# Performance work log

Measured on AMD Instinct MI355X. Metric: run time of the kernel, lower is better.

## Reference

```python
import jax, jax.numpy as jnp
import numpy as np

N = 50000
E = 800000
D = 128          # in_dim = hidden_dim = out_dim
H = 4            # heads
C = D // H       # per-head channels = 32
L = 3            # num_layers
SLOPE = 0.2
BN_EPS = 1e-5


def setup_inputs() -> dict:
    key = jax.random.key(0)
    ks = jax.random.split(key, 12)
    x = jax.random.normal(ks[0], (N, D), dtype=jnp.float32)
    ei = jax.random.randint(ks[1], (2, E), 0, N, dtype=jnp.int64)
    # remove accidental self loops (PyG removes then re-adds them)
    src, dst = ei[0], ei[1]
    src = jnp.where(src == dst, (src + 1) % N, src)
    edge_index = jnp.stack([src, dst])
    s = 1.0 / np.sqrt(D)
    Wl = jax.random.normal(ks[2], (L, D, D), dtype=jnp.float32) * s
    Wr = jax.random.normal(ks[3], (L, D, D), dtype=jnp.float32) * s
    att = jax.random.normal(ks[4], (L, H, C), dtype=jnp.float32) * (1.0 / np.sqrt(C))
    bias = jnp.zeros((L, D), dtype=jnp.float32)
    Wres = jax.random.normal(ks[5], (L, D, D), dtype=jnp.float32) * s
    gamma = jnp.ones((L, D), dtype=jnp.float32)
    beta = jnp.zeros((L, D), dtype=jnp.float32)
    W_out = jax.random.normal(ks[6], (D, D), dtype=jnp.float32) * s
    b_out = jnp.zeros((D,), dtype=jnp.float32)
    return {"x": x, "edge_index": edge_index, "Wl": Wl, "Wr": Wr, "att": att,
            "bias": bias, "Wres": Wres, "gamma": gamma, "beta": beta,
            "W_out": W_out, "b_out": b_out}


def _segment_softmax(scores, seg, num_segments):
    # scores: [E, H], seg: [E] dst ids
    m = jax.ops.segment_max(scores, seg, num_segments=num_segments)  # [N, H]
    ex = jnp.exp(scores - m[seg])
    denom = jax.ops.segment_sum(ex, seg, num_segments=num_segments)  # [N, H]
    return ex / denom[seg]


def _gatv2_layer(x, src, dst, Wl_, Wr_, att_, b_, Wres_):
    xl = (x @ Wl_).reshape(N, H, C)   # source-side transform
    xr = (x @ Wr_).reshape(N, H, C)   # target-side transform
    msg = xl[src]                      # [E, H, C]
    pre = jax.nn.leaky_relu(msg + xr[dst], SLOPE)
    e = jnp.einsum('ehc,hc->eh', pre, att_)          # [E, H]
    alpha = _segment_softmax(e, dst, N)              # [E, H]
    agg = jax.ops.segment_sum(alpha[..., None] * msg, dst, num_segments=N)
    return agg.reshape(N, D) + b_ + x @ Wres_


def _batch_norm(x, g, b):
    mu = jnp.mean(x, axis=0)
    var = jnp.mean(jnp.square(x - mu), axis=0)  # biased, as in torch BN
    return (x - mu) * jax.lax.rsqrt(var + BN_EPS) * g + b


def reference(x, edge_index, Wl, Wr, att, bias, Wres, gamma, beta, W_out, b_out):
    # add self loops once (same augmentation every layer)
    loops = jnp.arange(N, dtype=edge_index.dtype)
    src = jnp.concatenate([edge_index[0], loops])
    dst = jnp.concatenate([edge_index[1], loops])
    for i in range(L):
        x = _gatv2_layer(x, src, dst, Wl[i], Wr[i], att[i], bias[i], Wres[i])
        x = _batch_norm(x, gamma[i], beta[i])
        x = jax.nn.leaky_relu(x, SLOPE)
        # dropout = identity in eval
    return x @ W_out + b_out
```

## Files before the change

### kernel.cpp

```cpp
#include <hip/hip_runtime.h>
#include <hip/hip_bf16.h>

constexpr int N = 50000;
constexpr int E = 800000;
constexpr int D = 128;
constexpr int H = 4;
constexpr int C = 32;
constexpr int L = 3;
constexpr int E2 = E + N;
constexpr float SLOPE = 0.2f;
constexpr float BN_EPS = 1e-5f;
constexpr float LOG2E = 1.4426950408889634f;
constexpr int TILES = (N + 63) / 64;
constexpr int NPART = 32;

typedef __attribute__((ext_vector_type(8))) short bf16x8_t;
typedef __attribute__((ext_vector_type(4))) float f32x4_t;
typedef __attribute__((ext_vector_type(2))) float v2f;

using hbf = __hip_bfloat16;

__device__ __forceinline__ float fast_exp2(float x) { return __builtin_amdgcn_exp2f(x); }

__device__ __forceinline__ short f2bf(float v) {
    hbf h = __float2bfloat16(v);
    return *reinterpret_cast<short*>(&h);
}
__device__ __forceinline__ v2f bfpair_to_v2(unsigned int u) {
    v2f r;
    r.x = __uint_as_float(u << 16);
    r.y = __uint_as_float(u & 0xffff0000u);
    return r;
}

__global__ void count_kernel(const int* __restrict__ ei, int* __restrict__ counts,
                             int* __restrict__ rank) {
    int i = blockIdx.x * blockDim.x + threadIdx.x;
    if (i >= E2) return;
    int dst = (i < E) ? ei[E + i] : (i - E);
    rank[i] = atomicAdd(&counts[dst], 1);
}

__global__ __launch_bounds__(512) void scan_block_kernel(const int* __restrict__ counts,
                                                         int* __restrict__ row_ptr,
                                                         int* __restrict__ blk_sums) {
    __shared__ int s[512];
    int t = threadIdx.x;
    int i = blockIdx.x * 512 + t;
    int v = (i < N) ? counts[i] : 0;
    s[t] = v;
    __syncthreads();
    for (int off = 1; off < 512; off <<= 1) {
        int add = (t >= off) ? s[t - off] : 0;
        __syncthreads();
        s[t] += add;
        __syncthreads();
    }
    if (i < N) row_ptr[i] = s[t] - v;
    if (t == 511) blk_sums[blockIdx.x] = s[511];
}

__global__ __launch_bounds__(128) void scan_sums_kernel(int* __restrict__ blk, int nb) {
    __shared__ int s[128];
    int t = threadIdx.x;
    int v = (t < nb) ? blk[t] : 0;
    s[t] = v;
    __syncthreads();
    for (int off = 1; off < 128; off <<= 1) {
        int add = (t >= off) ? s[t - off] : 0;
        __syncthreads();
        s[t] += add;
        __syncthreads();
    }
    if (t < nb) blk[t] = s[t] - v;
}

__global__ void scan_add_kernel(int* __restrict__ row_ptr, const int* __restrict__ blk) {
    int i = blockIdx.x * blockDim.x + threadIdx.x;
    if (i < N) row_ptr[i] += blk[i >> 9];
    if (i == 0) row_ptr[N] = E2;
}

__global__ void scatter_kernel(const int* __restrict__ ei, const int* __restrict__ row_ptr,
                               const int* __restrict__ rank, int* __restrict__ col_idx) {
    int i = blockIdx.x * blockDim.x + threadIdx.x;
    if (i >= E2) return;
    int src, dst;
    if (i < E) { src = ei[i]; dst = ei[E + i]; }
    else       { src = i - E; dst = i - E; }
    col_idx[row_ptr[dst] + rank[i]] = src;
}

__global__ __launch_bounds__(256) void pack_w_kernel(
        const float* __restrict__ Wl, const float* __restrict__ Wr,
        const float* __restrict__ Wres, const float* __restrict__ Wout,
        hbf* __restrict__ Wph) {
    int gid = blockIdx.x * 256 + threadIdx.x;
    int mat = gid >> 14;
    int d = gid & 16383;
    const float* W;
    if (mat < 3)      W = Wl + (size_t)mat * 16384;
    else if (mat < 6) W = Wr + (size_t)(mat - 3) * 16384;
    else if (mat < 9) W = Wres + (size_t)(mat - 6) * 16384;
    else              W = Wout;
    int j = d & 7, lane = (d >> 3) & 63, nb = (d >> 9) & 7, ks = d >> 12;
    int k = ks * 32 + ((lane >> 4) * 8) + j;
    int n = nb * 16 + (lane & 15);
    Wph[gid] = __float2bfloat16(W[k * D + n]);
}

__global__ __launch_bounds__(256) void gemm3_mfma_kernel(
        const float* x, const float* __restrict__ sums,
        const float* __restrict__ gamma, const float* __restrict__ beta,
        const hbf* __restrict__ Wph,
        int mL, int mR, int mS, const float* __restrict__ bias,
        hbf* __restrict__ xl, hbf* __restrict__ xr, float* y) {
    __shared__ hbf xsh[64][136];
    __shared__ hbf xsl[64][136];
    __shared__ float ssl[2][128];
    int t = threadIdx.x;
    int wave = t >> 6;
    int lane = t & 63;
    int nb0 = wave * 2;
    int row0 = blockIdx.x * 64;

    if (sums && t < 128) {
        float sm = 0.f, s2 = 0.f;
#pragma unroll 8
        for (int p = 0; p < NPART; ++p) {
            sm += sums[p * 256 + t];
            s2 += sums[p * 256 + 128 + t];
        }
        float mean = sm * (1.0f / N);
        float var = fmaxf(s2 * (1.0f / N) - mean * mean, 0.f);
        float sc = gamma[t] * rsqrtf(var + BN_EPS);
        ssl[0][t] = sc;
        ssl[1][t] = beta[t] - mean * sc;
    }

    const bf16x8_t* B = (const bf16x8_t*)Wph;
    bf16x8_t bL[4][2], bR[4][2], bS[4][2];
#pragma unroll
    for (int ks = 0; ks < 4; ++ks)
#pragma unroll
        for (int j = 0; j < 2; ++j) {
            int bo = (ks * 8 + nb0 + j) * 64 + lane;
            bL[ks][j] = B[mL * 2048 + bo];
            bR[ks][j] = B[mR * 2048 + bo];
            bS[ks][j] = B[mS * 2048 + bo];
        }
    __syncthreads();

    int cg = (t & 31) * 4;
    {
        float sc_[4] = {1.f, 1.f, 1.f, 1.f}, sh_[4] = {0.f, 0.f, 0.f, 0.f};
        if (sums) {
#pragma unroll
            for (int j = 0; j < 4; ++j) { sc_[j] = ssl[0][cg + j]; sh_[j] = ssl[1][cg + j]; }
        }
        const float4* x4 = (const float4*)(x + (size_t)row0 * D);
        for (int i = t; i < 64 * 32; i += 256) {
            int r = i >> 5;
            float4 v = make_float4(0.f, 0.f, 0.f, 0.f);
            if (row0 + r < N) {
                v = x4[i];
                if (sums) {
                    v.x = fmaf(v.x, sc_[0], sh_[0]); v.x = fmaxf(v.x, SLOPE * v.x);
                    v.y = fmaf(v.y, sc_[1], sh_[1]); v.y = fmaxf(v.y, SLOPE * v.y);
                    v.z = fmaf(v.z, sc_[2], sh_[2]); v.z = fmaxf(v.z, SLOPE * v.z);
                    v.w = fmaf(v.w, sc_[3], sh_[3]); v.w = fmaxf(v.w, SLOPE * v.w);
                }
            }
            short h0 = f2bf(v.x), h1 = f2bf(v.y), h2 = f2bf(v.z), h3 = f2bf(v.w);
            float r0 = v.x - __uint_as_float(((unsigned)(unsigned short)h0) << 16);
            float r1 = v.y - __uint_as_float(((unsigned)(unsigned short)h1) << 16);
            float r2 = v.z - __uint_as_float(((unsigned)(unsigned short)h2) << 16);
            float r3 = v.w - __uint_as_float(((unsigned)(unsigned short)h3) << 16);
            short l0 = f2bf(r0), l1 = f2bf(r1), l2 = f2bf(r2), l3 = f2bf(r3);
            uint2 hp, lp;
            hp.x = (unsigned)(unsigned short)h0 | ((unsigned)(unsigned short)h1 << 16);
            hp.y = (unsigned)(unsigned short)h2 | ((unsigned)(unsigned short)h3 << 16);
            lp.x = (unsigned)(unsigned short)l0 | ((unsigned)(unsigned short)l1 << 16);
            lp.y = (unsigned)(unsigned short)l2 | ((unsigned)(unsigned short)l3 << 16);
            *(uint2*)&xsh[r][cg] = hp;
            *(uint2*)&xsl[r][cg] = lp;
        }
    }
    __syncthreads();

    int col = lane & 15;
    int koff = (lane >> 4) * 8;
    for (int mm = 0; mm < 4; ++mm) {
        int mrow = mm * 16 + (lane & 15);
        f32x4_t aL[2], aR[2], aS[2];
#pragma unroll
        for (int j = 0; j < 2; ++j) {
            aL[j] = (f32x4_t)0.f; aR[j] = (f32x4_t)0.f; aS[j] = (f32x4_t)0.f;
        }
#pragma unroll
        for (int ks = 0; ks < 4; ++ks) {
            bf16x8_t ah = *(const bf16x8_t*)&xsh[mrow][ks * 32 + koff];
            bf16x8_t al = *(const bf16x8_t*)&xsl[mrow][ks * 32 + koff];
#pragma unroll
            for (int j = 0; j < 2; ++j) {
                aL[j] = __builtin_amdgcn_mfma_f32_16x16x32_bf16(ah, bL[ks][j], aL[j], 0, 0, 0);
                aL[j] = __builtin_amdgcn_mfma_f32_16x16x32_bf16(al, bL[ks][j], aL[j], 0, 0, 0);
                aR[j] = __builtin_amdgcn_mfma_f32_16x16x32_bf16(ah, bR[ks][j], aR[j], 0, 0, 0);
                aR[j] = __builtin_amdgcn_mfma_f32_16x16x32_bf16(al, bR[ks][j], aR[j], 0, 0, 0);
                aS[j] = __builtin_amdgcn_mfma_f32_16x16x32_bf16(ah, bS[ks][j], aS[j], 0, 0, 0);
                aS[j] = __builtin_amdgcn_mfma_f32_16x16x32_bf16(al, bS[ks][j], aS[j], 0, 0, 0);
            }
        }
        int rowq = row0 + mm * 16 + (lane >> 4) * 4;
#pragma unroll
        for (int j = 0; j < 2; ++j) {
            int n = (nb0 + j) * 16 + col;
            float bv = bias[n];
#pragma unroll
            for (int r = 0; r < 4; ++r) {
                int row = rowq + r;
                if (row < N) {
                    xl[(size_t)row * D + n] = __float2bfloat16(aL[j][r]);
                    xr[(size_t)row * D + n] = __float2bfloat16(aR[j][r]);
                    y[(size_t)row * D + n]  = aS[j][r] + bv;
                }
            }
        }
    }
}

__global__ __launch_bounds__(256) void gemm_out_mfma_kernel(
        const float* __restrict__ x, const float* __restrict__ sums,
        const float* __restrict__ gamma, const float* __restrict__ beta,
        const hbf* __restrict__ Wph, const float* __restrict__ b,
        float* __restrict__ out) {
    __shared__ hbf xsh[64][136];
    __shared__ hbf xsl[64][136];
    __shared__ float ssl[2][128];
    int t = threadIdx.x;
    int wave = t >> 6;
    int lane = t & 63;
    int nb0 = wave * 2;
    int row0 = blockIdx.x * 64;

    if (t < 128) {
        float sm = 0.f, s2 = 0.f;
#pragma unroll 8
        for (int p = 0; p < NPART; ++p) {
            sm += sums[p * 256 + t];
            s2 += sums[p * 256 + 128 + t];
        }
        float mean = sm * (1.0f / N);
        float var = fmaxf(s2 * (1.0f / N) - mean * mean, 0.f);
        float sc = gamma[t] * rsqrtf(var + BN_EPS);
        ssl[0][t] = sc;
        ssl[1][t] = beta[t] - mean * sc;
    }

    const bf16x8_t* B = (const bf16x8_t*)Wph + 9 * 2048;
    bf16x8_t bW[4][2];
#pragma unroll
    for (int ks = 0; ks < 4; ++ks)
#pragma unroll
        for (int j = 0; j < 2; ++j)
            bW[ks][j] = B[(ks * 8 + nb0 + j) * 64 + lane];
    __syncthreads();

    int cg = (t & 31) * 4;
    {
        float sc_[4], sh_[4];
#pragma unroll
        for (int j = 0; j < 4; ++j) { sc_[j] = ssl[0][cg + j]; sh_[j] = ssl[1][cg + j]; }
        const float4* x4 = (const float4*)(x + (size_t)row0 * D);
        for (int i = t; i < 64 * 32; i += 256) {
            int r = i >> 5;
            float4 v = make_float4(0.f, 0.f, 0.f, 0.f);
            if (row0 + r < N) {
                v = x4[i];
                v.x = fmaf(v.x, sc_[0], sh_[0]); v.x = fmaxf(v.x, SLOPE * v.x);
                v.y = fmaf(v.y, sc_[1], sh_[1]); v.y = fmaxf(v.y, SLOPE * v.y);
                v.z = fmaf(v.z, sc_[2], sh_[2]); v.z = fmaxf(v.z, SLOPE * v.z);
                v.w = fmaf(v.w, sc_[3], sh_[3]); v.w = fmaxf(v.w, SLOPE * v.w);
            }
            short h0 = f2bf(v.x), h1 = f2bf(v.y), h2 = f2bf(v.z), h3 = f2bf(v.w);
            float r0 = v.x - __uint_as_float(((unsigned)(unsigned short)h0) << 16);
            float r1 = v.y - __uint_as_float(((unsigned)(unsigned short)h1) << 16);
            float r2 = v.z - __uint_as_float(((unsigned)(unsigned short)h2) << 16);
            float r3 = v.w - __uint_as_float(((unsigned)(unsigned short)h3) << 16);
            short l0 = f2bf(r0), l1 = f2bf(r1), l2 = f2bf(r2), l3 = f2bf(r3);
            uint2 hp, lp;
            hp.x = (unsigned)(unsigned short)h0 | ((unsigned)(unsigned short)h1 << 16);
            hp.y = (unsigned)(unsigned short)h2 | ((unsigned)(unsigned short)h3 << 16);
            lp.x = (unsigned)(unsigned short)l0 | ((unsigned)(unsigned short)l1 << 16);
            lp.y = (unsigned)(unsigned short)l2 | ((unsigned)(unsigned short)l3 << 16);
            *(uint2*)&xsh[r][cg] = hp;
            *(uint2*)&xsl[r][cg] = lp;
        }
    }
    __syncthreads();

    int col = lane & 15;
    int koff = (lane >> 4) * 8;
    for (int mm = 0; mm < 4; ++mm) {
        int mrow = mm * 16 + (lane & 15);
        f32x4_t acc[2];
        acc[0] = (f32x4_t)0.f; acc[1] = (f32x4_t)0.f;
#pragma unroll
        for (int ks = 0; ks < 4; ++ks) {
            bf16x8_t ah = *(const bf16x8_t*)&xsh[mrow][ks * 32 + koff];
            bf16x8_t al = *(const bf16x8_t*)&xsl[mrow][ks * 32 + koff];
#pragma unroll
            for (int j = 0; j < 2; ++j) {
                acc[j] = __builtin_amdgcn_mfma_f32_16x16x32_bf16(ah, bW[ks][j], acc[j], 0, 0, 0);
                acc[j] = __builtin_amdgcn_mfma_f32_16x16x32_bf16(al, bW[ks][j], acc[j], 0, 0, 0);
            }
        }
        int rowq = row0 + mm * 16 + (lane >> 4) * 4;
#pragma unroll
        for (int j = 0; j < 2; ++j) {
            int n = (nb0 + j) * 16 + col;
            float bv = b[n];
#pragma unroll
            for (int r = 0; r < 4; ++r) {
                int row = rowq + r;
                if (row < N) out[(size_t)row * D + n] = acc[j][r] + bv;
            }
        }
    }
}

__global__ __launch_bounds__(256) void gat_kernel(
        const hbf* __restrict__ xl, const hbf* __restrict__ xr,
        float* y, const int* __restrict__ row_ptr,
        const int* __restrict__ col_idx, const float* __restrict__ att,
        float* __restrict__ bn_part) {
    __shared__ float bs[8][132];
    __shared__ float bs2[8][132];
    int wave = threadIdx.x >> 6;
    int lane = threadIdx.x & 63;
    int e    = (lane >> 4) & 1;
    int sub  = lane & 15;
    int half = lane >> 5;
    int v = blockIdx.x * 8 + wave * 2 + half;
    const uint4* xlp = (const uint4*)xl;
    const uint4* xrp = (const uint4*)xr;
    uint4 xru = xrp[(size_t)v * 16 + sub];
    v2f xr_a = bfpair_to_v2(xru.x);
    v2f xr_b = bfpair_to_v2(xru.y);
    v2f xr_c = bfpair_to_v2(xru.z);
    v2f xr_d = bfpair_to_v2(xru.w);
    const float4* attf = (const float4*)att;
    float4 a4lo = attf[sub * 2];
    float4 a4hi = attf[sub * 2 + 1];
    v2f a_a; a_a.x = a4lo.x * LOG2E; a_a.y = a4lo.y * LOG2E;
    v2f a_b; a_b.x = a4lo.z * LOG2E; a_b.y = a4lo.w * LOG2E;
    v2f a_c; a_c.x = a4hi.x * LOG2E; a_c.y = a4hi.y * LOG2E;
    v2f a_d; a_d.x = a4hi.z * LOG2E; a_d.y = a4hi.w * LOG2E;
    int beg = row_ptr[v], end = row_ptr[v + 1];
    int d = end - beg;
    int dmax = max(d, __shfl_xor(d, 32));
    float l = 0.f;
    v2f acc_a = {0.f, 0.f};
    v2f acc_b = {0.f, 0.f};
    v2f acc_c = {0.f, 0.f};
    v2f acc_d = {0.f, 0.f};

    uint4 u0[2], u1[2];
    int c0[2], c1[2];
    u0[0] = xlp[(size_t)col_idx[min(beg + 0 + e, end - 1)] * 16 + sub];
    u0[1] = xlp[(size_t)col_idx[min(beg + 2 + e, end - 1)] * 16 + sub];
    u1[0] = xlp[(size_t)col_idx[min(beg + 4 + e, end - 1)] * 16 + sub];
    u1[1] = xlp[(size_t)col_idx[min(beg + 6 + e, end - 1)] * 16 + sub];
    c0[0] = col_idx[min(beg + 8 + e, end - 1)];
    c0[1] = col_idx[min(beg + 10 + e, end - 1)];
    c1[0] = col_idx[min(beg + 12 + e, end - 1)];
    c1[1] = col_idx[min(beg + 14 + e, end - 1)];

    int off = 0;
    auto process4 = [&](uint4 (&buf)[2], int (&cid)[2]) {
        v2f xa0 = bfpair_to_v2(buf[0].x);
        v2f xb0 = bfpair_to_v2(buf[0].y);
        v2f xc0 = bfpair_to_v2(buf[0].z);
        v2f xd0 = bfpair_to_v2(buf[0].w);
        v2f xa1 = bfpair_to_v2(buf[1].x);
        v2f xb1 = bfpair_to_v2(buf[1].y);
        v2f xc1 = bfpair_to_v2(buf[1].z);
        v2f xd1 = bfpair_to_v2(buf[1].w);
        buf[0] = xlp[(size_t)cid[0] * 16 + sub];
        buf[1] = xlp[(size_t)cid[1] * 16 + sub];
        cid[0] = col_idx[min(beg + off + 16 + e, end - 1)];
        cid[1] = col_idx[min(beg + off + 18 + e, end - 1)];

        v2f pa = xa0 + xr_a, pb = xb0 + xr_b;
        v2f pc = xc0 + xr_c, pd = xd0 + xr_d;
        pa = __builtin_elementwise_max(pa, pa * SLOPE);
        pb = __builtin_elementwise_max(pb, pb * SLOPE);
        pc = __builtin_elementwise_max(pc, pc * SLOPE);
        pd = __builtin_elementwise_max(pd, pd * SLOPE);
        v2f t0 = pa * a_a;
        t0 = pb * a_b + t0;
        t0 = pc * a_c + t0;
        t0 = pd * a_d + t0;
        pa = xa1 + xr_a; pb = xb1 + xr_b;
        pc = xc1 + xr_c; pd = xd1 + xr_d;
        pa = __builtin_elementwise_max(pa, pa * SLOPE);
        pb = __builtin_elementwise_max(pb, pb * SLOPE);
        pc = __builtin_elementwise_max(pc, pc * SLOPE);
        pd = __builtin_elementwise_max(pd, pd * SLOPE);
        v2f t1 = pa * a_a;
        t1 = pb * a_b + t1;
        t1 = pc * a_c + t1;
        t1 = pd * a_d + t1;
        float s0 = t0.x + t0.y;
        float s1 = t1.x + t1.y;
        s0 += __shfl_xor(s0, 1);  s1 += __shfl_xor(s1, 1);
        s0 += __shfl_xor(s0, 2);  s1 += __shfl_xor(s1, 2);
        float w0 = fast_exp2(s0);
        float w1 = fast_exp2(s1);
        w0 = (off + e < d) ? w0 : 0.f;
        w1 = (off + 2 + e < d) ? w1 : 0.f;
        l += w0 + w1;
        acc_a = xa0 * w0 + acc_a;
        acc_b = xb0 * w0 + acc_b;
        acc_c = xc0 * w0 + acc_c;
        acc_d = xd0 * w0 + acc_d;
        acc_a = xa1 * w1 + acc_a;
        acc_b = xb1 * w1 + acc_b;
        acc_c = xc1 * w1 + acc_c;
        acc_d = xd1 * w1 + acc_d;
    };

    while (true) {
        process4(u0, c0);
        off += 4;
        if (off >= dmax) break;
        process4(u1, c1);
        off += 4;
        if (off >= dmax) break;
    }
    l += __shfl_xor(l, 16);
    acc_a.x += __shfl_xor(acc_a.x, 16); acc_a.y += __shfl_xor(acc_a.y, 16);
    acc_b.x += __shfl_xor(acc_b.x, 16); acc_b.y += __shfl_xor(acc_b.y, 16);
    acc_c.x += __shfl_xor(acc_c.x, 16); acc_c.y += __shfl_xor(acc_c.y, 16);
    acc_d.x += __shfl_xor(acc_d.x, 16); acc_d.y += __shfl_xor(acc_d.y, 16);
    if (e == 0) {
        float rl = 1.f / l;
        size_t o = (size_t)v * 32 + sub * 2;
        float4 y0 = ((const float4*)y)[o];
        float4 y1 = ((const float4*)y)[o + 1];
        y0.x = fmaf(acc_a.x, rl, y0.x);
        y0.y = fmaf(acc_a.y, rl, y0.y);
        y0.z = fmaf(acc_b.x, rl, y0.z);
        y0.w = fmaf(acc_b.y, rl, y0.w);
        y1.x = fmaf(acc_c.x, rl, y1.x);
        y1.y = fmaf(acc_c.y, rl, y1.y);
        y1.z = fmaf(acc_d.x, rl, y1.z);
        y1.w = fmaf(acc_d.y, rl, y1.w);
        ((float4*)y)[o] = y0;
        ((float4*)y)[o + 1] = y1;
        int rrow = wave * 2 + half;
        int cb = sub * 8;
        bs[rrow][cb + 0] = y0.x;  bs2[rrow][cb + 0] = y0.x * y0.x;
        bs[rrow][cb + 1] = y0.y;  bs2[rrow][cb + 1] = y0.y * y0.y;
        bs[rrow][cb + 2] = y0.z;  bs2[rrow][cb + 2] = y0.z * y0.z;
        bs[rrow][cb + 3] = y0.w;  bs2[rrow][cb + 3] = y0.w * y0.w;
        bs[rrow][cb + 4] = y1.x;  bs2[rrow][cb + 4] = y1.x * y1.x;
        bs[rrow][cb + 5] = y1.y;  bs2[rrow][cb + 5] = y1.y * y1.y;
        bs[rrow][cb + 6] = y1.z;  bs2[rrow][cb + 6] = y1.z * y1.z;
        bs[rrow][cb + 7] = y1.w;  bs2[rrow][cb + 7] = y1.w * y1.w;
    }
    __syncthreads();
    int t = threadIdx.x;
    if (t < 128) {
        float a = 0.f, b2 = 0.f;
#pragma unroll
        for (int r = 0; r < 8; ++r) {
            a  += bs[r][t];
            b2 += bs2[r][t];
        }
        float* part = bn_part + (size_t)(blockIdx.x & (NPART - 1)) * 256;
        atomicAdd(&part[t], a);
        atomicAdd(&part[128 + t], b2);
    }
}

extern "C" void kernel_launch(void* const* d_in, const int* in_sizes, int n_in,
                              void* d_out, int out_size, void* d_ws, size_t ws_size,
                              hipStream_t stream) {
    const float* x_in  = (const float*)d_in[0];
    const int*   ei    = (const int*)d_in[1];
    const float* Wl    = (const float*)d_in[2];
    const float* Wr    = (const float*)d_in[3];
    const float* att   = (const float*)d_in[4];
    const float* bias  = (const float*)d_in[5];
    const float* Wres  = (const float*)d_in[6];
    const float* gamma = (const float*)d_in[7];
    const float* beta  = (const float*)d_in[8];
    const float* Wout  = (const float*)d_in[9];
    const float* bout  = (const float*)d_in[10];
    float* out = (float*)d_out;

    char* ws = (char*)d_ws;
    size_t off = 0;
    auto alloc = [&](size_t bytes) {
        void* p = ws + off;
        off = (off + bytes + 255) & ~(size_t)255;
        return p;
    };
    hbf*   xl       = (hbf*)alloc((size_t)N * D * sizeof(hbf));
    hbf*   xr       = (hbf*)alloc((size_t)N * D * sizeof(hbf));
    float* y        = (float*)alloc((size_t)N * D * sizeof(float));
    hbf*   Wph      = (hbf*)alloc((size_t)10 * D * D * sizeof(hbf));
    int*   row_ptr  = (int*)alloc((size_t)(N + 1) * sizeof(int));
    int*   col_idx  = (int*)alloc((size_t)E2 * sizeof(int));
    int*   counts   = (int*)alloc((size_t)N * sizeof(int));
    int*   rank     = (int*)alloc((size_t)E2 * sizeof(int));
    int*   blk_sums = (int*)alloc(128 * sizeof(int));
    float* sums     = (float*)alloc((size_t)3 * NPART * 256 * sizeof(float));

    const int NB = (N + 511) / 512;

    (void)hipMemsetAsync(counts, 0, (size_t)N * sizeof(int), stream);
    (void)hipMemsetAsync(sums, 0, (size_t)3 * NPART * 256 * sizeof(float), stream);
    count_kernel<<<(E2 + 255) / 256, 256, 0, stream>>>(ei, counts, rank);
    pack_w_kernel<<<10 * 16384 / 256, 256, 0, stream>>>(Wl, Wr, Wres, Wout, Wph);
    scan_block_kernel<<<NB, 512, 0, stream>>>(counts, row_ptr, blk_sums);
    scan_sums_kernel<<<1, 128, 0, stream>>>(blk_sums, NB);
    scan_add_kernel<<<(N + 255) / 256, 256, 0, stream>>>(row_ptr, blk_sums);
    scatter_kernel<<<(E2 + 255) / 256, 256, 0, stream>>>(ei, row_ptr, rank, col_idx);

    for (int i = 0; i < L; ++i) {
        const float* xin = (i == 0) ? x_in : y;
        const float* sm  = (i == 0) ? nullptr : sums + (size_t)(i - 1) * NPART * 256;
        const float* ga  = (i == 0) ? nullptr : gamma + (size_t)(i - 1) * D;
        const float* be  = (i == 0) ? nullptr : beta + (size_t)(i - 1) * D;
        gemm3_mfma_kernel<<<TILES, 256, 0, stream>>>(xin, sm, ga, be, Wph,
                                                     i, 3 + i, 6 + i,
                                                     bias + (size_t)i * D, xl, xr, y);
        gat_kernel<<<N / 8, 256, 0, stream>>>(xl, xr, y, row_ptr, col_idx,
                                              att + (size_t)i * H * C,
                                              sums + (size_t)i * NPART * 256);
    }

    gemm_out_mfma_kernel<<<TILES, 256, 0, stream>>>(y, sums + (size_t)2 * NPART * 256,
                                                    gamma + (size_t)2 * D,
                                                    beta + (size_t)2 * D, Wph, bout, out);
}
```

Baseline: 371.4 us.

## Sort nodes by in-degree bins so GAT waves process similar-degree nodes

Adds a counting-sort pass that builds a permutation of nodes grouped by in-degree (capped at 64 bins), and the GAT kernel maps each half-wave to a node via this permutation. The intent is to cut intra-wave divergence, since each wave loops to the max degree of its two nodes, and to balance work across blocks. The cost is three small extra kernels plus an indirect node lookup. Scattered node order also reduces locality for the xr reads and y writes.

```diff
diff --git a/kernel.cpp b/kernel.cpp
--- a/kernel.cpp
+++ b/kernel.cpp
@@ -13,6 +13,7 @@
 constexpr float LOG2E = 1.4426950408889634f;
 constexpr int TILES = (N + 63) / 64;
 constexpr int NPART = 32;
+constexpr int NBINS = 64;
 
 typedef __attribute__((ext_vector_type(8))) short bf16x8_t;
 typedef __attribute__((ext_vector_type(4))) float f32x4_t;
@@ -89,6 +90,50 @@
     if (i < E) { src = ei[i]; dst = ei[E + i]; }
     else       { src = i - E; dst = i - E; }
     col_idx[row_ptr[dst] + rank[i]] = src;
+}
+
+__global__ __launch_bounds__(256) void deg_rank_kernel(const int* __restrict__ counts,
+                                                       int* __restrict__ ghist,
+                                                       int* __restrict__ rankb) {
+    __shared__ int lh[NBINS];
+    __shared__ int lbase[NBINS];
+    int t = threadIdx.x;
+    if (t < NBINS) lh[t] = 0;
+    __syncthreads();
+    int v = blockIdx.x * 256 + t;
+    int b = 0, lr = 0;
+    if (v < N) {
+        b = min(counts[v], NBINS - 1);
+        lr = atomicAdd(&lh[b], 1);
+    }
+    __syncthreads();
+    if (t < NBINS && lh[t] > 0) lbase[t] = atomicAdd(&ghist[t], lh[t]);
+    __syncthreads();
+    if (v < N) rankb[v] = lbase[b] + lr;
+}
+
+__global__ __launch_bounds__(64) void bin_scan_kernel(const int* __restrict__ ghist,
+                                                      int* __restrict__ binbase) {
+    __shared__ int s[NBINS];
+    int t = threadIdx.x;
+    int v = ghist[t];
+    s[t] = v;
+    __syncthreads();
+    for (int off = 1; off < NBINS; off <<= 1) {
+        int add = (t >= off) ? s[t - off] : 0;
+        __syncthreads();
+        s[t] += add;
+        __syncthreads();
+    }
+    binbase[t] = s[t] - v;
+}
+
+__global__ void perm_kernel(const int* __restrict__ counts, const int* __restrict__ rankb,
+                            const int* __restrict__ binbase, int* __restrict__ perm) {
+    int v = blockIdx.x * 256 + threadIdx.x;
+    if (v >= N) return;
+    int b = min(counts[v], NBINS - 1);
+    perm[binbase[b] + rankb[v]] = v;
 }
 
 __global__ __launch_bounds__(256) void pack_w_kernel(
@@ -333,7 +378,7 @@
         const hbf* __restrict__ xl, const hbf* __restrict__ xr,
         float* y, const int* __restrict__ row_ptr,
         const int* __restrict__ col_idx, const float* __restrict__ att,
-        float* __restrict__ bn_part) {
+        float* __restrict__ bn_part, const int* __restrict__ perm) {
     __shared__ float bs[8][132];
     __shared__ float bs2[8][132];
     int wave = threadIdx.x >> 6;
@@ -341,7 +386,7 @@
     int e    = (lane >> 4) & 1;
     int sub  = lane & 15;
     int half = lane >> 5;
-    int v = blockIdx.x * 8 + wave * 2 + half;
+    int v = perm[blockIdx.x * 8 + wave * 2 + half];
     const uint4* xlp = (const uint4*)xl;
     const uint4* xrp = (const uint4*)xr;
     uint4 xru = xrp[(size_t)v * 16 + sub];
@@ -513,17 +558,25 @@
     hbf*   Wph      = (hbf*)alloc((size_t)10 * D * D * sizeof(hbf));
     int*   row_ptr  = (int*)alloc((size_t)(N + 1) * sizeof(int));
     int*   col_idx  = (int*)alloc((size_t)E2 * sizeof(int));
-    int*   counts   = (int*)alloc((size_t)N * sizeof(int));
+    int*   counts   = (int*)alloc((size_t)(N + 2 * NBINS) * sizeof(int));
     int*   rank     = (int*)alloc((size_t)E2 * sizeof(int));
+    int*   rankb    = (int*)alloc((size_t)N * sizeof(int));
+    int*   perm     = (int*)alloc((size_t)N * sizeof(int));
     int*   blk_sums = (int*)alloc(128 * sizeof(int));
     float* sums     = (float*)alloc((size_t)3 * NPART * 256 * sizeof(float));
 
+    int* ghist   = counts + N;
+    int* binbase = counts + N + NBINS;
     const int NB = (N + 511) / 512;
-
-    (void)hipMemsetAsync(counts, 0, (size_t)N * sizeof(int), stream);
+    const int NBLK = (N + 255) / 256;
+
+    (void)hipMemsetAsync(counts, 0, (size_t)(N + 2 * NBINS) * sizeof(int), stream);
     (void)hipMemsetAsync(sums, 0, (size_t)3 * NPART * 256 * sizeof(float), stream);
     count_kernel<<<(E2 + 255) / 256, 256, 0, stream>>>(ei, counts, rank);
     pack_w_kernel<<<10 * 16384 / 256, 256, 0, stream>>>(Wl, Wr, Wres, Wout, Wph);
+    deg_rank_kernel<<<NBLK, 256, 0, stream>>>(counts, ghist, rankb);
+    bin_scan_kernel<<<1, NBINS, 0, stream>>>(ghist, binbase);
+    perm_kernel<<<NBLK, 256, 0, stream>>>(counts, rankb, binbase, perm);
     scan_block_kernel<<<NB, 512, 0, stream>>>(counts, row_ptr, blk_sums);
     scan_sums_kernel<<<1, 128, 0, stream>>>(blk_sums, NB);
     scan_add_kernel<<<(N + 255) / 256, 256, 0, stream>>>(row_ptr, blk_sums);
@@ -539,7 +592,7 @@
                                                      bias + (size_t)i * D, xl, xr, y);
         gat_kernel<<<N / 8, 256, 0, stream>>>(xl, xr, y, row_ptr, col_idx,
                                               att + (size_t)i * H * C,
-                                              sums + (size_t)i * NPART * 256);
+                                              sums + (size_t)i * NPART * 256, perm);
     }
 
     gemm_out_mfma_kernel<<<TILES, 256, 0, stream>>>(y, sums + (size_t)2 * NPART * 256,
```

Result: no change. 375.9 us (+1.2%).
